# Kernel tuning notes

Measured on AMD Instinct MI355X. Metric: run time of the kernel, lower is better.

Reference implementation:

```python
import jax, jax.numpy as jnp
import numpy as np

NK, TH, SHARP, IMW, IMH = 9, 80.0, 2.0, 640.0, 480.0
NOOBJ, OBJ, COORD, CLS_SCALE, SIL = 1.0, 5.0, 1.0, 1.0, 0.6
NA, NC = 1, 13

def corner_conf(pr, gt):
    # pr, gt: [..., 9, 2] normalized corner coords
    scale = jnp.array([IMW, IMH], dtype=pr.dtype)
    d = (gt - pr) * scale
    dist = jnp.sqrt(jnp.sum(d * d, axis=-1))
    c = (jnp.exp(SHARP * (1.0 - dist / TH)) - 1.0) / (np.exp(SHARP) - 1.0)
    return jnp.where(dist < TH, c, 0.0).mean(axis=-1)

def build_targets(pc, target, nH, nW):
    # pc: [nB, nA*nH*nW, 9, 2] detached predicted corners (layout anchor-major, matching torch flatten)
    nB = target.shape[0]
    nL = 2 * NK + 3
    tgt = target.reshape(nB, 50, nL)
    # break on first slot with coord==0 -> valid prefix
    valid = jnp.cumprod((tgt[:, :, 1] != 0).astype(jnp.int32), axis=1).astype(bool)
    gt_c = tgt[:, :, 1:1 + 2 * NK].reshape(nB, 50, NK, 2)
    confs = corner_conf(pc[:, None], gt_c[:, :, None])  # [nB, 50, nAnch]
    cur = jnp.max(jnp.where(valid[:, :, None], confs, 0.0), axis=1)  # running max over targets
    conf_mask = jnp.where(cur > SIL, 0.0, NOOBJ).reshape(nB, NA, nH, nW)
    gi = (tgt[:, :, 1] * nW).astype(jnp.int32)  # int() truncation, coords in (0,1)
    gj = (tgt[:, :, 2] * nH).astype(jnp.int32)
    coord_mask = jnp.zeros((nB, NA, nH, nW), target.dtype)
    cls_mask = jnp.zeros((nB, NA, nH, nW), target.dtype)
    tcls = jnp.zeros((nB, NA, nH, nW), target.dtype)
    b = jnp.arange(nB)
    for t in range(50):  # fixed 50-slot buffer; sequential overwrite preserved
        git = jnp.where(valid[:, t], gi[:, t], nW)  # invalid -> OOB index, dropped
        gjt = gj[:, t]
        coord_mask = coord_mask.at[b, 0, gjt, git].set(1.0, mode='drop')
        conf_mask = conf_mask.at[b, 0, gjt, git].set(OBJ, mode='drop')
        cls_mask = cls_mask.at[b, 0, gjt, git].set(1.0, mode='drop')
        tcls = tcls.at[b, 0, gjt, git].set(tgt[:, t, 0], mode='drop')
    return coord_mask, conf_mask, cls_mask, tcls

def forward(output, distiled_target, target):
    nB, _, nH, nW = output.shape
    out = output.reshape(nB, NA, 19 + NC, nH, nW)
    coords = jnp.concatenate([jax.nn.sigmoid(out[:, :, :2]), out[:, :, 2:18]], axis=2)
    conf = jax.nn.sigmoid(out[:, :, 18])
    cls_logits = out[:, :, 19:]  # [nB, nA, nC, nH, nW]
    gx = jnp.arange(nW, dtype=output.dtype)
    gy = jnp.arange(nH, dtype=output.dtype)
    px = (coords[:, :, 0::2] + gx[None, None, None, None, :]) / nW  # [nB,NA,9,nH,nW]
    py = (coords[:, :, 1::2] + gy[None, None, None, :, None]) / nH
    pc = jnp.stack([px, py], axis=-1)  # [nB,NA,9,nH,nW,2]
    pc = jnp.transpose(pc, (0, 1, 3, 4, 2, 5)).reshape(nB, NA * nH * nW, NK, 2)
    pc = jax.lax.stop_gradient(pc)  # torch uses .data (detached) for build_targets
    coord_mask, conf_mask, cls_mask, tcls = build_targets(pc, target, nH, nW)
    # distilled (teacher) targets replace build_targets' tx*/ty*/tconf
    dt = distiled_target.reshape(nB, NA, 19 + NC, nH, nW)
    tcoords = jnp.concatenate([jax.nn.sigmoid(dt[:, :, :2]), dt[:, :, 2:18]], axis=2)
    tconf = jax.nn.sigmoid(dt[:, :, 18])
    cm = coord_mask[:, :, None]  # broadcast over 18 coord channels
    loss_coord = COORD * 0.5 * jnp.sum(((coords - tcoords) * cm) ** 2)
    loss_conf = 0.5 * jnp.sum(((conf - tconf) * jnp.sqrt(conf_mask)) ** 2)
    logp = jax.nn.log_softmax(cls_logits, axis=2)
    ce = -jnp.take_along_axis(logp, tcls.astype(jnp.int32)[:, :, None], axis=2)[:, :, 0]
    loss_cls = CLS_SCALE * jnp.sum(cls_mask * ce)  # CrossEntropyLoss(size_average=False) on masked cells
    return loss_coord + loss_conf + loss_cls

def setup_inputs():
    key = jax.random.key(0)
    k1, k2, k3, k4 = jax.random.split(key, 4)
    nB, nH, nW = 16, 76, 76
    output = jax.random.normal(k1, (nB, NA * (19 + NC), nH, nW), dtype=jnp.float32)
    distiled_target = jax.random.normal(k2, (nB, NA * (19 + NC), nH, nW), dtype=jnp.float32)
    nL = 2 * NK + 3
    target = jax.random.uniform(k3, (nB, 50 * nL), dtype=jnp.float32, minval=0.02, maxval=0.98)
    cls_col = jax.random.randint(k4, (nB, 50), 0, NC).astype(jnp.float32)
    target = target.at[:, 0::nL].set(cls_col)
    target = target.at[:, 20 * nL:].set(0.0)  # 20 valid objects per image
    return {"output": output, "distiled_target": distiled_target, "target": target}

def reference(output, distiled_target, target):
    return forward(output, distiled_target, target)
```

## Files before the change

### kernel.cpp

```cpp
#include <hip/hip_runtime.h>
#include <math.h>

#define NB    16
#define NH    76
#define NW    76
#define NCELL (NH * NW)
#define NITEM (NB * NCELL)
#define NCH   32
#define NKP   9
#define NCLS  13
#define NT    50
#define NLROW 21
#define BLOCK 128
#define GRID  (NITEM / BLOCK)

#define INV_EM1 0.15651764274966565f
#define SX 8.421052631578947f
#define SY 6.315789473684211f

__device__ __forceinline__ float sigmoidf_(float x) {
    return 1.0f / (1.0f + __expf(-x));
}

__global__ __launch_bounds__(BLOCK) void loss_main(
    const float* __restrict__ out,
    const float* __restrict__ dt,
    const float* __restrict__ tgt,
    float* __restrict__ outp,
    float* __restrict__ partials,
    int use_ws)
{
    __shared__ float2 s_g[2][NT][NKP];
    __shared__ int    s_gij[2][NT];
    __shared__ int    s_cls[2][NT];
    __shared__ int    s_nv[2];
    __shared__ float  swsum[BLOCK / 64];

    const int tid  = threadIdx.x;
    const int idx0 = blockIdx.x * BLOCK;
    const int b0   = idx0 / NCELL;
    const int b1   = (idx0 + BLOCK - 1) / NCELL;

    for (int u = tid; u < 2 * NT; u += BLOCK) {
        const int bi = u / NT;
        const int t  = u - bi * NT;
        const int bb = bi ? b1 : b0;
        const float* __restrict__ r = tgt + (size_t)bb * (NT * NLROW) + t * NLROW;
        #pragma unroll
        for (int k = 0; k < NKP; k++)
            s_g[bi][t][k] = make_float2(r[1 + 2 * k] * 640.0f, r[2 + 2 * k] * 480.0f);
        const int gi = (int)(r[1] * (float)NW);
        const int gj = (int)(r[2] * (float)NH);
        s_gij[bi][t] = (gj << 8) | gi;
        s_cls[bi][t] = min(max((int)r[0], 0), NCLS - 1);
    }
    {
        const int wv = tid >> 6, ln = tid & 63;
        const int bb = wv ? b1 : b0;
        const float x0 = (ln < NT) ? tgt[(size_t)bb * (NT * NLROW) + ln * NLROW + 1] : 0.0f;
        const unsigned long long zmask = __ballot(x0 == 0.0f);
        if (ln == 0) s_nv[wv] = (int)__ffsll((unsigned long long)zmask) - 1;
    }
    __syncthreads();

    const int idx  = idx0 + tid;
    const int b    = idx / NCELL;
    const int cell = idx - b * NCELL;
    const int j    = cell / NW;
    const int i    = cell - j * NW;
    const int bi   = (b != b0);
    const int myg  = (j << 8) | i;
    const int nv   = s_nv[bi];
    const float fi = (float)i, fj = (float)j;

    const float* __restrict__ ob = out + (size_t)b * NCH * NCELL + cell;
    const float* __restrict__ db = dt  + (size_t)b * NCH * NCELL + cell;

    float ax[NKP], ay[NKP], px[NKP], py[NKP];
    #pragma unroll
    for (int k = 0; k < NKP; k++) {
        float cx = ob[(2 * k)     * NCELL];
        float cy = ob[(2 * k + 1) * NCELL];
        if (k == 0) { cx = sigmoidf_(cx); cy = sigmoidf_(cy); }
        ax[k] = cx; ay[k] = cy;
        px[k] = (cx + fi) * SX;
        py[k] = (cy + fj) * SY;
    }
    const float conf  = sigmoidf_(ob[18 * NCELL]);
    const float tconf = sigmoidf_(db[18 * NCELL]);

    float cur9 = 0.0f;
    int flag = 0, tcls = 0;
    for (int t = 0; t < nv; t++) {
        const int g = s_gij[bi][t];
        if (g == myg) { flag = 1; tcls = s_cls[bi][t]; }
        float s = 0.0f;
        #pragma unroll
        for (int k = 0; k < NKP; k++) {
            const float2 gp = s_g[bi][t][k];
            const float dx = gp.x - px[k];
            const float dy = gp.y - py[k];
            const float d2 = __builtin_fmaf(dx, dx, dy * dy);
            if (__any(d2 < 6400.0f)) {
                const float dist = __builtin_amdgcn_sqrtf(d2);
                const float c = (__expf(__builtin_fmaf(dist, -0.025f, 2.0f)) - 1.0f) * INV_EM1;
                s += (d2 < 6400.0f) ? c : 0.0f;
            }
        }
        cur9 = fmaxf(cur9, s);
    }

    float total;
    {
        const float cmask = flag ? 5.0f : (cur9 > 5.4f ? 0.0f : 1.0f);
        const float dcf = conf - tconf;
        total = 0.5f * dcf * dcf * cmask;
    }

    if (flag) {
        float cl = 0.0f;
        #pragma unroll
        for (int k = 0; k < NKP; k++) {
            float bx = db[(2 * k)     * NCELL];
            float by = db[(2 * k + 1) * NCELL];
            if (k == 0) { bx = sigmoidf_(bx); by = sigmoidf_(by); }
            const float d1 = ax[k] - bx;
            const float d2_ = ay[k] - by;
            cl += d1 * d1 + d2_ * d2_;
        }
        total += 0.5f * cl;

        float cvv[NCLS];
        float mx = -1e30f, vt = 0.0f;
        #pragma unroll
        for (int c2 = 0; c2 < NCLS; c2++) {
            const float v = ob[(19 + c2) * NCELL];
            cvv[c2] = v;
            mx = fmaxf(mx, v);
            vt = (c2 == tcls) ? v : vt;
        }
        float se = 0.0f;
        #pragma unroll
        for (int c2 = 0; c2 < NCLS; c2++) se += __expf(cvv[c2] - mx);
        total += mx + __logf(se) - vt;
    }

    #pragma unroll
    for (int off = 32; off > 0; off >>= 1)
        total += __shfl_down(total, off, 64);
    if ((tid & 63) == 0) swsum[tid >> 6] = total;
    __syncthreads();
    if (tid == 0) {
        float sm = swsum[0];
        #pragma unroll
        for (int w = 1; w < BLOCK / 64; w++) sm += swsum[w];
        if (use_ws) partials[blockIdx.x] = sm;
        else        atomicAdd(outp, sm);
    }
}

__global__ __launch_bounds__(256) void reduce_partials(
    const float* __restrict__ p, float* __restrict__ outp)
{
    __shared__ float w[4];
    float s = 0.0f;
    for (int k = threadIdx.x; k < GRID; k += 256) s += p[k];
    #pragma unroll
    for (int off = 32; off > 0; off >>= 1)
        s += __shfl_down(s, off, 64);
    if ((threadIdx.x & 63) == 0) w[threadIdx.x >> 6] = s;
    __syncthreads();
    if (threadIdx.x == 0) outp[0] = w[0] + w[1] + w[2] + w[3];
}

extern "C" void kernel_launch(void* const* d_in, const int* in_sizes, int n_in,
                              void* d_out, int out_size, void* d_ws, size_t ws_size,
                              hipStream_t stream) {
    const float* out_p = (const float*)d_in[0];
    const float* dt_p  = (const float*)d_in[1];
    const float* tgt_p = (const float*)d_in[2];
    const int use_ws = (d_ws != nullptr && ws_size >= GRID * sizeof(float));
    float* partials = (float*)d_ws;

    loss_main<<<GRID, BLOCK, 0, stream>>>(out_p, dt_p, tgt_p, (float*)d_out,
                                          partials, use_ws);
    if (use_ws)
        reduce_partials<<<1, 256, 0, stream>>>(partials, (float*)d_out);
}
```

Baseline: 83.63 us.

## Process two cells per thread with wave-level y-range culling of targets

```diff
diff --git a/kernel.cpp b/kernel.cpp
--- a/kernel.cpp
+++ b/kernel.cpp
@@ -12,11 +12,14 @@
 #define NT    50
 #define NLROW 21
 #define BLOCK 128
-#define GRID  (NITEM / BLOCK)
+#define NPAIR (NITEM / 2)
+#define GRID  (NPAIR / BLOCK)
 
 #define INV_EM1 0.15651764274966565f
 #define SX 8.421052631578947f
 #define SY 6.315789473684211f
+#define C0 2.885390081777927f
+#define C1 0.036067376022224085f
 
 __device__ __forceinline__ float sigmoidf_(float x) {
     return 1.0f / (1.0f + __expf(-x));
@@ -36,97 +39,133 @@
     __shared__ int    s_nv[2];
     __shared__ float  swsum[BLOCK / 64];
 
-    const int tid  = threadIdx.x;
-    const int idx0 = blockIdx.x * BLOCK;
-    const int b0   = idx0 / NCELL;
-    const int b1   = (idx0 + BLOCK - 1) / NCELL;
+    const int tid    = threadIdx.x;
+    const int pair0  = blockIdx.x * BLOCK;
+    const int cell00 = pair0 * 2;
+    const int b0     = cell00 / NCELL;
+    const int b1     = (cell00 + 2 * BLOCK - 1) / NCELL;
 
     for (int u = tid; u < 2 * NT; u += BLOCK) {
-        const int bi = u / NT;
-        const int t  = u - bi * NT;
-        const int bb = bi ? b1 : b0;
+        const int bsel = u / NT;
+        const int t    = u - bsel * NT;
+        const int bb   = bsel ? b1 : b0;
         const float* __restrict__ r = tgt + (size_t)bb * (NT * NLROW) + t * NLROW;
         #pragma unroll
         for (int k = 0; k < NKP; k++)
-            s_g[bi][t][k] = make_float2(r[1 + 2 * k] * 640.0f, r[2 + 2 * k] * 480.0f);
+            s_g[bsel][t][k] = make_float2(r[1 + 2 * k] * 640.0f, r[2 + 2 * k] * 480.0f);
         const int gi = (int)(r[1] * (float)NW);
         const int gj = (int)(r[2] * (float)NH);
-        s_gij[bi][t] = (gj << 8) | gi;
-        s_cls[bi][t] = min(max((int)r[0], 0), NCLS - 1);
+        s_gij[bsel][t] = (gj << 8) | gi;
+        s_cls[bsel][t] = min(max((int)r[0], 0), NCLS - 1);
     }
     {
         const int wv = tid >> 6, ln = tid & 63;
         const int bb = wv ? b1 : b0;
         const float x0 = (ln < NT) ? tgt[(size_t)bb * (NT * NLROW) + ln * NLROW + 1] : 0.0f;
         const unsigned long long zmask = __ballot(x0 == 0.0f);
-        if (ln == 0) s_nv[wv] = (int)__ffsll((unsigned long long)zmask) - 1;
+        if (ln == 0) s_nv[wv] = (int)__ffsll(zmask) - 1;
     }
     __syncthreads();
 
-    const int idx  = idx0 + tid;
-    const int b    = idx / NCELL;
-    const int cell = idx - b * NCELL;
-    const int j    = cell / NW;
-    const int i    = cell - j * NW;
-    const int bi   = (b != b0);
-    const int myg  = (j << 8) | i;
-    const int nv   = s_nv[bi];
-    const float fi = (float)i, fj = (float)j;
-
-    const float* __restrict__ ob = out + (size_t)b * NCH * NCELL + cell;
-    const float* __restrict__ db = dt  + (size_t)b * NCH * NCELL + cell;
-
-    float ax[NKP], ay[NKP], px[NKP], py[NKP];
+    const int p     = pair0 + tid;
+    const int c1g   = 2 * p;
+    const int b     = c1g / NCELL;
+    const int cell1 = c1g - b * NCELL;
+    const int j     = cell1 / NW;
+    const int i1    = cell1 - j * NW;
+    const int bi    = (b != b0);
+    const int nv    = s_nv[bi];
+    const int myg1  = (j << 8) | i1;
+    const int myg2  = myg1 + 1;
+    const float fj  = (float)j;
+
+    const float* __restrict__ ob = out + (size_t)b * NCH * NCELL + cell1;
+    const float* __restrict__ db = dt  + (size_t)b * NCH * NCELL + cell1;
+
+    float ax1[NKP], ay1[NKP], px1[NKP], py1[NKP];
+    float ax2[NKP], ay2[NKP], px2[NKP], py2[NKP];
+    float ymn = 1e30f, ymx = -1e30f;
     #pragma unroll
     for (int k = 0; k < NKP; k++) {
-        float cx = ob[(2 * k)     * NCELL];
-        float cy = ob[(2 * k + 1) * NCELL];
-        if (k == 0) { cx = sigmoidf_(cx); cy = sigmoidf_(cy); }
-        ax[k] = cx; ay[k] = cy;
-        px[k] = (cx + fi) * SX;
-        py[k] = (cy + fj) * SY;
-    }
-    const float conf  = sigmoidf_(ob[18 * NCELL]);
-    const float tconf = sigmoidf_(db[18 * NCELL]);
-
-    float cur9 = 0.0f;
-    int flag = 0, tcls = 0;
+        float2 vx = *(const float2*)(ob + (2 * k)     * NCELL);
+        float2 vy = *(const float2*)(ob + (2 * k + 1) * NCELL);
+        float cx1 = vx.x, cx2 = vx.y, cy1 = vy.x, cy2 = vy.y;
+        if (k == 0) { cx1 = sigmoidf_(cx1); cx2 = sigmoidf_(cx2);
+                      cy1 = sigmoidf_(cy1); cy2 = sigmoidf_(cy2); }
+        ax1[k] = cx1; ax2[k] = cx2; ay1[k] = cy1; ay2[k] = cy2;
+        px1[k] = (cx1 + (float)i1) * SX;  px2[k] = (cx2 + (float)(i1 + 1)) * SX;
+        py1[k] = (cy1 + fj) * SY;         py2[k] = (cy2 + fj) * SY;
+        ymn = fminf(ymn, fminf(py1[k], py2[k]));
+        ymx = fmaxf(ymx, fmaxf(py1[k], py2[k]));
+    }
+    const float2 vcf  = *(const float2*)(ob + 18 * NCELL);
+    const float2 vtcf = *(const float2*)(db + 18 * NCELL);
+    const float conf1 = sigmoidf_(vcf.x),  conf2 = sigmoidf_(vcf.y);
+    const float tcf1  = sigmoidf_(vtcf.x), tcf2  = sigmoidf_(vtcf.y);
+
+    #pragma unroll
+    for (int off = 32; off > 0; off >>= 1) {
+        ymn = fminf(ymn, __shfl_xor(ymn, off, 64));
+        ymx = fmaxf(ymx, __shfl_xor(ymx, off, 64));
+    }
+    const float ylo = ymn - 80.0f, yhi = ymx + 80.0f;
+
+    float cur1 = 0.0f, cur2 = 0.0f;
+    int flag1 = 0, flag2 = 0, tc1 = 0, tc2 = 0;
     for (int t = 0; t < nv; t++) {
         const int g = s_gij[bi][t];
-        if (g == myg) { flag = 1; tcls = s_cls[bi][t]; }
-        float s = 0.0f;
+        if (g == myg1) { flag1 = 1; tc1 = s_cls[bi][t]; }
+        if (g == myg2) { flag2 = 1; tc2 = s_cls[bi][t]; }
+        float s1 = 0.0f, s2 = 0.0f;
         #pragma unroll
         for (int k = 0; k < NKP; k++) {
             const float2 gp = s_g[bi][t][k];
-            const float dx = gp.x - px[k];
-            const float dy = gp.y - py[k];
-            const float d2 = __builtin_fmaf(dx, dx, dy * dy);
-            if (__any(d2 < 6400.0f)) {
-                const float dist = __builtin_amdgcn_sqrtf(d2);
-                const float c = (__expf(__builtin_fmaf(dist, -0.025f, 2.0f)) - 1.0f) * INV_EM1;
-                s += (d2 < 6400.0f) ? c : 0.0f;
+            if (gp.y > ylo && gp.y < yhi) {
+                const float dx1 = gp.x - px1[k], dy1 = gp.y - py1[k];
+                const float dx2 = gp.x - px2[k], dy2 = gp.y - py2[k];
+                const float d21 = __builtin_fmaf(dx1, dx1, dy1 * dy1);
+                const float d22 = __builtin_fmaf(dx2, dx2, dy2 * dy2);
+                if (__any(fminf(d21, d22) < 6400.0f)) {
+                    const float c1 = (__builtin_amdgcn_exp2f(
+                        __builtin_fmaf(__builtin_amdgcn_sqrtf(d21), -C1, C0)) - 1.0f) * INV_EM1;
+                    const float c2 = (__builtin_amdgcn_exp2f(
+                        __builtin_fmaf(__builtin_amdgcn_sqrtf(d22), -C1, C0)) - 1.0f) * INV_EM1;
+                    s1 += (d21 < 6400.0f) ? c1 : 0.0f;
+                    s2 += (d22 < 6400.0f) ? c2 : 0.0f;
+                }
             }
         }
-        cur9 = fmaxf(cur9, s);
+        cur1 = fmaxf(cur1, s1);
+        cur2 = fmaxf(cur2, s2);
     }
 
     float total;
     {
-        const float cmask = flag ? 5.0f : (cur9 > 5.4f ? 0.0f : 1.0f);
-        const float dcf = conf - tconf;
-        total = 0.5f * dcf * dcf * cmask;
-    }
-
-    if (flag) {
+        const float cm1 = flag1 ? 5.0f : (cur1 > 5.4f ? 0.0f : 1.0f);
+        const float cm2 = flag2 ? 5.0f : (cur2 > 5.4f ? 0.0f : 1.0f);
+        const float d1 = conf1 - tcf1, d2 = conf2 - tcf2;
+        total = 0.5f * (d1 * d1 * cm1 + d2 * d2 * cm2);
+    }
+
+    #pragma unroll
+    for (int it = 0; it < 2; it++) {
+        const int   fl   = it ? flag2 : flag1;
+        if (!fl) continue;
+        const int   tcls = it ? tc2 : tc1;
+        const float* obi = ob + it;
+        const float* dbi = db + it;
+        const float* axi = it ? ax2 : ax1;
+        const float* ayi = it ? ay2 : ay1;
+
         float cl = 0.0f;
         #pragma unroll
         for (int k = 0; k < NKP; k++) {
-            float bx = db[(2 * k)     * NCELL];
-            float by = db[(2 * k + 1) * NCELL];
+            float bx = dbi[(2 * k)     * NCELL];
+            float by = dbi[(2 * k + 1) * NCELL];
             if (k == 0) { bx = sigmoidf_(bx); by = sigmoidf_(by); }
-            const float d1 = ax[k] - bx;
-            const float d2_ = ay[k] - by;
-            cl += d1 * d1 + d2_ * d2_;
+            const float e1 = axi[k] - bx;
+            const float e2 = ayi[k] - by;
+            cl += e1 * e1 + e2 * e2;
         }
         total += 0.5f * cl;
 
@@ -134,7 +173,7 @@
         float mx = -1e30f, vt = 0.0f;
         #pragma unroll
         for (int c2 = 0; c2 < NCLS; c2++) {
-            const float v = ob[(19 + c2) * NCELL];
+            const float v = obi[(19 + c2) * NCELL];
             cvv[c2] = v;
             mx = fmaxf(mx, v);
             vt = (c2 == tcls) ? v : vt;
```

After: 93.40 us. +11.7%, slower.
